# Performance work log

Measured on AMD Instinct MI355X. Metric: run time of the kernel, lower is better.

The kernel has to match this reference:

```python
import jax, jax.numpy as jnp
import numpy as np
from jax import lax

SFREQ = 250.0
ORDER = 4
BANDS = [(4.0, 8.0), (8.0, 12.0), (12.0, 16.0), (16.0, 20.0), (20.0, 24.0), (24.0, 28.0), (28.0, 32.0), (32.0, 36.0), (36.0, 40.0)]
KLEN = int(SFREQ // 2)
if KLEN % 2 == 0:
    KLEN += 1  # 125 taps, odd -> same-length output with pad K//2


def _butter_bandpass(order, low, high, sfreq):
    # numpy reimplementation of scipy.signal.butter(order, [low,high]/nyq, btype='band')
    nyq = sfreq / 2.0
    fs = 2.0
    warped = 2.0 * fs * np.tan(np.pi * np.array([low, high]) / nyq / fs)
    m = np.arange(-order + 1, order, 2)
    p = -np.exp(1j * np.pi * m / (2 * order))  # analog Butterworth LP prototype poles
    k = 1.0
    bw = warped[1] - warped[0]
    wo = np.sqrt(warped[0] * warped[1])
    p_lp = p * bw / 2.0
    p_bp = np.concatenate([p_lp + np.sqrt(p_lp ** 2 - wo ** 2), p_lp - np.sqrt(p_lp ** 2 - wo ** 2)])
    z_bp = np.zeros(order, dtype=complex)
    k_bp = k * bw ** order
    fs2 = 2.0 * fs  # bilinear transform
    z_d = (fs2 + z_bp) / (fs2 - z_bp)
    p_d = (fs2 + p_bp) / (fs2 - p_bp)
    z_d = np.append(z_d, -np.ones(len(p_bp) - len(z_bp)))
    k_d = k_bp * np.real(np.prod(fs2 - z_bp) / np.prod(fs2 - p_bp))
    b = np.real(k_d * np.poly(z_d))
    a = np.real(np.poly(p_d))
    return b, a


def _make_kernel(low, high):
    # IIR impulse response (centered impulse, as in the torch module), Hann window, L1 normalize
    b, a = _butter_bandpass(ORDER, low, high, SFREQ)
    x = np.zeros(KLEN)
    x[KLEN // 2] = 1.0
    h = np.zeros(KLEN)
    for n in range(KLEN):
        s = 0.0
        for i in range(len(b)):
            if n - i >= 0:
                s += b[i] * x[n - i]
        for j in range(1, len(a)):
            if n - j >= 0:
                s -= a[j] * h[n - j]
        h[n] = s / a[0]
    nn = np.arange(KLEN)
    h = h * (0.5 - 0.5 * np.cos(2.0 * np.pi * nn / (KLEN - 1)))  # symmetric Hann
    return h / np.sum(np.abs(h))


def setup_inputs() -> dict:
    key = jax.random.key(0)
    x = jax.random.normal(key, (64, 64, 1000), dtype=jnp.float32)  # (B, C, T) EEG
    kernels = jnp.asarray(np.stack([_make_kernel(lo, hi) for lo, hi in BANDS]), dtype=jnp.float32)  # (n_bands, K)
    return {"x": x, "kernels": kernels}


def reference(x, kernels):
    # out[b, i, c, t] = cross-correlation of channel c with band-i kernel (torch Conv1d semantics)
    B, C, T = x.shape
    nb, K = kernels.shape
    pad = K // 2
    x2 = x.reshape(B * C, 1, T)
    w = kernels[:, None, :]  # (n_bands, 1, K)
    y = lax.conv_general_dilated(x2, w, (1,), [(pad, pad)], dimension_numbers=("NCH", "OIH", "NCH"))
    return y.reshape(B, C, nb, T).transpose(0, 2, 1, 3)  # (B, n_bands, C, T)
```

## Files before the change

### kernel.cpp

```cpp
#include <hip/hip_runtime.h>
#include <hip/hip_bf16.h>


#define T_LEN    1000
#define NB       9
#define KP       128
#define S_COPY   1160
#define SLOTS    145
#define STG_W    264

typedef __attribute__((ext_vector_type(8))) short short8;
typedef __attribute__((ext_vector_type(4))) float f32x4;

__device__ __forceinline__ unsigned int f2bf(float f) {
    union { __hip_bfloat16 h; unsigned short u; } cv;
    cv.h = __float2bfloat16(f);
    return (unsigned int)cv.u;
}

__global__ __launch_bounds__(256) void prep_taps(const float* __restrict__ kern,
                                                 unsigned short* __restrict__ kwb) {
    const int t = threadIdx.x;
    #pragma unroll
    for (int i = 0; i < 8; ++i) {
        int idx = t + 256 * i;
        int band = idx >> 7, k = idx & 127;
        float v = (band < NB && k < 125) ? kern[band * 125 + k] : 0.f;
        kwb[idx] = (unsigned short)f2bf(v);
    }
}

__global__ __launch_bounds__(256) void fbank_mfma(
    const float* __restrict__ x,
    const unsigned short* __restrict__ kwb,
    float* __restrict__ out)
{
    __shared__ unsigned short xs[8 * S_COPY];

    const int tid = threadIdx.x;
    const int bid = blockIdx.x;
    const int bc  = ((bid & 7) << 9) + (bid >> 3);
    const int b   = bc >> 6, c = bc & 63;
    const float* xrow = x + (size_t)bc * T_LEN;

    {
        const int r = tid >> 5, q0 = tid & 31;
        #pragma unroll
        for (int i = 0; i < 5; ++i) {
            int q = q0 + 32 * i;
            if (q < SLOTS) {
                int idx0 = 8 * q + r - 64;
                unsigned int d[4];
                #pragma unroll
                for (int e2 = 0; e2 < 4; ++e2) {
                    int i0 = idx0 + 2 * e2, i1 = i0 + 1;
                    float v0 = ((unsigned)i0 < T_LEN) ? xrow[i0] : 0.f;
                    float v1 = ((unsigned)i1 < T_LEN) ? xrow[i1] : 0.f;
                    d[e2] = f2bf(v0) | (f2bf(v1) << 16);
                }
                *reinterpret_cast<uint4*>(&xs[r * S_COPY + 8 * q]) =
                    make_uint4(d[0], d[1], d[2], d[3]);
            }
        }
    }

    const int lane = tid & 63;
    const int wid  = tid >> 6;
    const int n = lane & 15, g = lane >> 4;

    short8 bt[4];
    #pragma unroll
    for (int kk = 0; kk < 4; ++kk)
        bt[kk] = *reinterpret_cast<const short8*>(kwb + n * KP + kk * 32 + g * 8);

    __syncthreads();

    const int t0w = wid << 8;
    const int rl  = (n + 2) & 7;
    const char* xsb = reinterpret_cast<const char*>(xs);
    const int LB = 2 * (1159 * rl + 2 + n + 8 * g + t0w);

    short8 F[8];
    #pragma unroll
    for (int u = 0; u < 6; ++u)
        F[u] = *reinterpret_cast<const short8*>(xsb + LB + 32 * u);

    f32x4 acc[16];
    #pragma unroll
    for (int m = 0; m < 16; ++m) {
        F[(m + 6) & 7] = *reinterpret_cast<const short8*>(xsb + LB + 32 * (m + 6));
        f32x4 a = {0.f, 0.f, 0.f, 0.f};
        #pragma unroll
        for (int kk = 0; kk < 4; ++kk)
            a = __builtin_amdgcn_mfma_f32_16x16x32_bf16(F[(m + 2 * kk) & 7], bt[kk], a, 0, 0, 0);
        acc[m] = a;
    }

    float* stg = reinterpret_cast<float*>(xs);
    for (int w = 0; w < 4; ++w) {
        __syncthreads();
        if (wid == w) {
            if (n < NB) {
                #pragma unroll
                for (int m = 0; m < 16; ++m)
                    *reinterpret_cast<f32x4*>(stg + n * STG_W + 16 * m + 4 * g) = acc[m];
            }
            const int tl = 4 * lane;
            const bool ok = (t0w + tl + 4 <= T_LEN);
            #pragma unroll
            for (int i = 0; i < NB; ++i) {
                f32x4 v = *reinterpret_cast<const f32x4*>(stg + i * STG_W + tl);
                if (ok)
                    *reinterpret_cast<f32x4*>(
                        out + ((size_t)(b * NB + i) * 64 + c) * T_LEN + t0w + tl) = v;
            }
        }
    }
}

extern "C" void kernel_launch(void* const* d_in, const int* in_sizes, int n_in,
                              void* d_out, int out_size, void* d_ws, size_t ws_size,
                              hipStream_t stream) {
    const float* x    = (const float*)d_in[0];
    const float* kern = (const float*)d_in[1];
    float* out = (float*)d_out;
    unsigned short* kwb = (unsigned short*)d_ws;

    prep_taps<<<1, 256, 0, stream>>>(kern, kwb);
    fbank_mfma<<<64 * 64, 256, 0, stream>>>(x, kwb, out);
}
```

Measured before the change: 56.20 us.

## Loop blocks over four rows each and parallelize output staging across waves

The grid shrinks from 4096 to 1024 blocks and each block loops over four (batch, channel) rows. This amortizes the per-block tap loads and launch overhead. The output epilogue now stages two waves' results at a time and has all four waves store the rows, replacing the serial one-wave-at-a-time staging. The cost is that loads of the next row no longer overlap with other blocks' compute the way extra resident blocks did, and shared memory grows to 18.7 KB, which may lower occupancy.

```diff
diff --git a/kernel.cpp b/kernel.cpp
--- a/kernel.cpp
+++ b/kernel.cpp
@@ -2,12 +2,13 @@
 #include <hip/hip_bf16.h>
 
 
-#define T_LEN    1000
-#define NB       9
-#define KP       128
-#define S_COPY   1160
-#define SLOTS    145
-#define STG_W    264
+#define T_LEN      1000
+#define NB         9
+#define KP         128
+#define S_COPY     1160
+#define SLOTS      145
+#define STG_STRIDE 520
+#define SMEM_BYTES (NB * STG_STRIDE * 4)
 
 typedef __attribute__((ext_vector_type(8))) short short8;
 typedef __attribute__((ext_vector_type(4))) float f32x4;
@@ -35,35 +36,12 @@
     const unsigned short* __restrict__ kwb,
     float* __restrict__ out)
 {
-    __shared__ unsigned short xs[8 * S_COPY];
+    __shared__ char smem[SMEM_BYTES];
+    unsigned short* xs = reinterpret_cast<unsigned short*>(smem);
+    float* stg = reinterpret_cast<float*>(smem);
 
-    const int tid = threadIdx.x;
-    const int bid = blockIdx.x;
-    const int bc  = ((bid & 7) << 9) + (bid >> 3);
-    const int b   = bc >> 6, c = bc & 63;
-    const float* xrow = x + (size_t)bc * T_LEN;
-
-    {
-        const int r = tid >> 5, q0 = tid & 31;
-        #pragma unroll
-        for (int i = 0; i < 5; ++i) {
-            int q = q0 + 32 * i;
-            if (q < SLOTS) {
-                int idx0 = 8 * q + r - 64;
-                unsigned int d[4];
-                #pragma unroll
-                for (int e2 = 0; e2 < 4; ++e2) {
-                    int i0 = idx0 + 2 * e2, i1 = i0 + 1;
-                    float v0 = ((unsigned)i0 < T_LEN) ? xrow[i0] : 0.f;
-                    float v1 = ((unsigned)i1 < T_LEN) ? xrow[i1] : 0.f;
-                    d[e2] = f2bf(v0) | (f2bf(v1) << 16);
-                }
-                *reinterpret_cast<uint4*>(&xs[r * S_COPY + 8 * q]) =
-                    make_uint4(d[0], d[1], d[2], d[3]);
-            }
-        }
-    }
-
+    const int tid  = threadIdx.x;
+    const int bid  = blockIdx.x;
     const int lane = tid & 63;
     const int wid  = tid >> 6;
     const int n = lane & 15, g = lane >> 4;
@@ -73,47 +51,79 @@
     for (int kk = 0; kk < 4; ++kk)
         bt[kk] = *reinterpret_cast<const short8*>(kwb + n * KP + kk * 32 + g * 8);
 
-    __syncthreads();
-
     const int t0w = wid << 8;
     const int rl  = (n + 2) & 7;
     const char* xsb = reinterpret_cast<const char*>(xs);
     const int LB = 2 * (1159 * rl + 2 + n + 8 * g + t0w);
 
-    short8 F[8];
-    #pragma unroll
-    for (int u = 0; u < 6; ++u)
-        F[u] = *reinterpret_cast<const short8*>(xsb + LB + 32 * u);
+    for (int it = 0; it < 4; ++it) {
+        const int bc = (it << 10) + bid;
+        const int b  = bc >> 6, c = bc & 63;
+        const float* xrow = x + (size_t)bc * T_LEN;
 
-    f32x4 acc[16];
-    #pragma unroll
-    for (int m = 0; m < 16; ++m) {
-        F[(m + 6) & 7] = *reinterpret_cast<const short8*>(xsb + LB + 32 * (m + 6));
-        f32x4 a = {0.f, 0.f, 0.f, 0.f};
+        __syncthreads();
+
+        {
+            const int r = tid >> 5, q0 = tid & 31;
+            #pragma unroll
+            for (int i = 0; i < 5; ++i) {
+                int q = q0 + 32 * i;
+                if (q < SLOTS) {
+                    int idx0 = 8 * q + r - 64;
+                    unsigned int d[4];
+                    #pragma unroll
+                    for (int e2 = 0; e2 < 4; ++e2) {
+                        int i0 = idx0 + 2 * e2, i1 = i0 + 1;
+                        float v0 = ((unsigned)i0 < T_LEN) ? xrow[i0] : 0.f;
+                        float v1 = ((unsigned)i1 < T_LEN) ? xrow[i1] : 0.f;
+                        d[e2] = f2bf(v0) | (f2bf(v1) << 16);
+                    }
+                    *reinterpret_cast<uint4*>(&xs[r * S_COPY + 8 * q]) =
+                        make_uint4(d[0], d[1], d[2], d[3]);
+                }
+            }
+        }
+        __syncthreads();
+
+        f32x4 acc[16];
+        short8 F[8];
         #pragma unroll
-        for (int kk = 0; kk < 4; ++kk)
-            a = __builtin_amdgcn_mfma_f32_16x16x32_bf16(F[(m + 2 * kk) & 7], bt[kk], a, 0, 0, 0);
-        acc[m] = a;
-    }
+        for (int u = 0; u < 6; ++u)
+            F[u] = *reinterpret_cast<const short8*>(xsb + LB + 32 * u);
+        #pragma unroll
+        for (int m = 0; m < 16; ++m) {
+            F[(m + 6) & 7] = *reinterpret_cast<const short8*>(xsb + LB + 32 * (m + 6));
+            f32x4 a = {0.f, 0.f, 0.f, 0.f};
+            #pragma unroll
+            for (int kk = 0; kk < 4; ++kk)
+                a = __builtin_amdgcn_mfma_f32_16x16x32_bf16(F[(m + 2 * kk) & 7], bt[kk], a, 0, 0, 0);
+            acc[m] = a;
+        }
 
-    float* stg = reinterpret_cast<float*>(xs);
-    for (int w = 0; w < 4; ++w) {
         __syncthreads();
-        if (wid == w) {
-            if (n < NB) {
+
+        #pragma unroll
+        for (int h = 0; h < 2; ++h) {
+            if ((wid >> 1) == h && n < NB) {
+                const int toff = (wid & 1) << 8;
                 #pragma unroll
                 for (int m = 0; m < 16; ++m)
-                    *reinterpret_cast<f32x4*>(stg + n * STG_W + 16 * m + 4 * g) = acc[m];
+                    *reinterpret_cast<f32x4*>(stg + n * STG_STRIDE + toff + 16 * m + 4 * g) = acc[m];
             }
-            const int tl = 4 * lane;
-            const bool ok = (t0w + tl + 4 <= T_LEN);
-            #pragma unroll
-            for (int i = 0; i < NB; ++i) {
-                f32x4 v = *reinterpret_cast<const f32x4*>(stg + i * STG_W + tl);
-                if (ok)
+            __syncthreads();
+            const int q0 = wid * 5;
+            const int qe = (wid == 3) ? 18 : q0 + 5;
+            for (int q = q0; q < qe; ++q) {
+                const int band = q >> 1, part = q & 1;
+                const int tloc = (h << 9) + (part << 8) + (lane << 2);
+                if (tloc + 4 <= T_LEN) {
+                    f32x4 v = *reinterpret_cast<const f32x4*>(
+                        stg + band * STG_STRIDE + (part << 8) + (lane << 2));
                     *reinterpret_cast<f32x4*>(
-                        out + ((size_t)(b * NB + i) * 64 + c) * T_LEN + t0w + tl) = v;
+                        out + ((size_t)(b * NB + band) * 64 + c) * T_LEN + tloc) = v;
+                }
             }
+            if (h == 0) __syncthreads();
         }
     }
 }
@@ -127,5 +137,5 @@
     unsigned short* kwb = (unsigned short*)d_ws;
 
     prep_taps<<<1, 256, 0, stream>>>(kern, kwb);
-    fbank_mfma<<<64 * 64, 256, 0, stream>>>(x, kwb, out);
+    fbank_mfma<<<1024, 256, 0, stream>>>(x, kwb, out);
 }
```

Result: slower. 72.72 us (+29.4%).
